# Optimization experiments

Measured on AMD Instinct MI355X. Metric: run time of the kernel, lower is better.

Reference implementation:

```python
import jax, jax.numpy as jnp
import numpy as np
import math

B, T_IN, T_COND, D, H, W = 2, 2048, 1024, 1024, 16, 512
HD = D // H
NEG = -1e9


def setup_inputs() -> dict:
    key = jax.random.key(0)
    ks = jax.random.split(key, 6)
    scale = 0.02
    x = jax.random.normal(ks[0], (B, T_IN, D), dtype=jnp.float32)
    condition = jax.random.normal(ks[1], (B, T_COND, D), dtype=jnp.float32)
    end_inds = jax.random.randint(ks[2], (B,), W, min(T_IN, T_COND), dtype=jnp.int32)
    in_proj_w = jax.random.normal(ks[3], (3 * D, D), dtype=jnp.float32) * scale
    in_proj_b = jnp.zeros((3 * D,), dtype=jnp.float32)
    out_w = jax.random.normal(ks[4], (D, D), dtype=jnp.float32) * scale
    out_b = jnp.zeros((D,), dtype=jnp.float32)
    return {"x": x, "condition": condition, "end_inds": end_inds,
            "in_proj_w": in_proj_w, "in_proj_b": in_proj_b,
            "out_w": out_w, "out_b": out_b}


def _window_mask(end_inds, t_in, t_cond):
    # allowed keys: index in [end - W, end) within each of the two segments
    e = end_inds[:, None].astype(jnp.int32)
    idx_in = jnp.arange(t_in, dtype=jnp.int32)[None, :]
    idx_c = jnp.arange(t_cond, dtype=jnp.int32)[None, :]
    m_in = (idx_in >= e - W) & (idx_in < e)
    m_c = (idx_c >= e - W) & (idx_c < e)
    return jnp.concatenate([m_in, m_c], axis=1)  # (B, S)


def reference(x, condition, end_inds, in_proj_w, in_proj_b, out_w, out_b):
    inp = jnp.concatenate([x, condition], axis=1)          # (B, S, D)
    S = inp.shape[1]
    qkv = inp @ in_proj_w.T + in_proj_b                     # (B, S, 3D)
    q, k, v = jnp.split(qkv, 3, axis=-1)
    # (B, H, S, HD)
    q = q.reshape(B, S, H, HD).transpose(0, 2, 1, 3)
    k = k.reshape(B, S, H, HD).transpose(0, 2, 1, 3)
    v = v.reshape(B, S, H, HD).transpose(0, 2, 1, 3)
    scores = jnp.einsum('bhqd,bhkd->bhqk', q, k) / math.sqrt(HD)
    mask = _window_mask(end_inds, x.shape[1], condition.shape[1])  # (B, S)
    scores = jnp.where(mask[:, None, None, :], scores, NEG)
    attn = jax.nn.softmax(scores, axis=-1)
    out = jnp.einsum('bhqk,bhkd->bhqd', attn, v)            # (B, H, S, HD)
    out = out.transpose(0, 2, 1, 3).reshape(B, S, D)
    return out @ out_w.T + out_b
```

## Files before the change

kernel.cpp:

```cpp
#include <hip/hip_runtime.h>
#include <stdint.h>

#define TIN   2048
#define TCOND 1024
#define SEQ   3072
#define NB    2
#define NH    16
#define DM    1024
#define HDIM  64
#define WIN   512
#define MROWS (NB*SEQ)
#define NQKV  (3*DM)

typedef float  floatx4 __attribute__((ext_vector_type(4)));
typedef short  bf16x8  __attribute__((ext_vector_type(8)));

__device__ __forceinline__ unsigned short f2bf(float f) {
    unsigned int u = __float_as_uint(f);
    u += 0x7fffu + ((u >> 16) & 1u);
    return (unsigned short)(u >> 16);
}

__device__ __forceinline__ unsigned int pack2bf(float a, float b) {
    return (unsigned int)f2bf(a) | ((unsigned int)f2bf(b) << 16);
}

__device__ __forceinline__ void gl2lds16(const void* g, void* l) {
    __builtin_amdgcn_global_load_lds(
        (const __attribute__((address_space(1))) unsigned int*)g,
        (__attribute__((address_space(3))) unsigned int*)l, 16, 0, 0);
}

__global__ __launch_bounds__(256) void pack_inp(const float* __restrict__ x,
                                                const float* __restrict__ cond,
                                                unsigned short* __restrict__ inp) {
    int v = blockIdx.x * 256 + threadIdx.x;
    int m  = v >> 8;
    int d4 = v & 255;
    int bb = (m >= SEQ) ? 1 : 0;
    int s  = m - bb * SEQ;
    const float* src = (s < TIN)
        ? x    + ((size_t)(bb * TIN   + s)        ) * DM + d4 * 4
        : cond + ((size_t)(bb * TCOND + (s - TIN))) * DM + d4 * 4;
    float4 f = *(const float4*)src;
    ushort4 u;
    u.x = f2bf(f.x); u.y = f2bf(f.y); u.z = f2bf(f.z); u.w = f2bf(f.w);
    *(ushort4*)(inp + (size_t)v * 4) = u;
}

__global__ __launch_bounds__(256) void cast_w(const float* __restrict__ w_in,
                                              const float* __restrict__ w_out,
                                              unsigned short* __restrict__ wi_bf,
                                              unsigned short* __restrict__ wo_bf) {
    int v = blockIdx.x * 256 + threadIdx.x;
    const float* src; unsigned short* dst; int idx;
    if (v < 786432) { src = w_in;  dst = wi_bf; idx = v; }
    else            { src = w_out; dst = wo_bf; idx = v - 786432; }
    float4 f = *(const float4*)(src + (size_t)idx * 4);
    ushort4 u;
    u.x = f2bf(f.x); u.y = f2bf(f.y); u.z = f2bf(f.z); u.w = f2bf(f.w);
    *(ushort4*)(dst + (size_t)idx * 4) = u;
}

template<int EPI>
__global__ __launch_bounds__(256) void gemm_bt(
        const unsigned short* __restrict__ A, const unsigned short* __restrict__ Bt,
        int M, int N, int K,
        const float* __restrict__ bias,
        unsigned short* __restrict__ q_ws, unsigned short* __restrict__ k_ws,
        unsigned short* __restrict__ vt_ws, float* __restrict__ outp) {
    __shared__ unsigned short smem[2 * 128 * 64];
    unsigned short* As = smem;
    unsigned short* Bs = smem + 128 * 64;
    const int tid  = threadIdx.x;
    const int wave = tid >> 6, lane = tid & 63;
    const int quad = lane >> 4, c16 = lane & 15;
    const int wr = wave >> 1, wc = wave & 1;
    const int m0 = blockIdx.y * 128, n0 = blockIdx.x * 128;

    floatx4 acc[4][4];
#pragma unroll
    for (int i = 0; i < 4; i++)
#pragma unroll
        for (int j = 0; j < 4; j++) acc[i][j] = (floatx4){0.f, 0.f, 0.f, 0.f};

    for (int k0 = 0; k0 < K; k0 += 64) {
        __syncthreads();
#pragma unroll
        for (int i = 0; i < 4; i++) {
            int flat = i * 256 + tid;
            int pr = flat >> 3, cp = flat & 7;
            gl2lds16(A + (size_t)(m0 + pr) * K + k0 + ((cp ^ (pr & 7)) << 3),
                     &As[(i * 256 + wave * 64) * 8]);
        }
#pragma unroll
        for (int i = 0; i < 4; i++) {
            int flat = i * 256 + tid;
            int pr = flat >> 3, cp = flat & 7;
            gl2lds16(Bt + (size_t)(n0 + pr) * K + k0 + ((cp ^ (pr & 7)) << 3),
                     &Bs[(i * 256 + wave * 64) * 8]);
        }
        __syncthreads();
#pragma unroll
        for (int kk = 0; kk < 2; kk++) {
            bf16x8 af[4], bfr[4];
#pragma unroll
            for (int t = 0; t < 4; t++) {
                int ra = wr * 64 + t * 16 + c16;
                int rb = wc * 64 + t * 16 + c16;
                af[t]  = *(const bf16x8*)&As[ra * 64 + (((kk * 4 + quad) ^ (ra & 7)) << 3)];
                bfr[t] = *(const bf16x8*)&Bs[rb * 64 + (((kk * 4 + quad) ^ (rb & 7)) << 3)];
            }
#pragma unroll
            for (int mt = 0; mt < 4; mt++)
#pragma unroll
                for (int nt = 0; nt < 4; nt++)
                    acc[mt][nt] = __builtin_amdgcn_mfma_f32_16x16x32_bf16(
                        af[mt], bfr[nt], acc[mt][nt], 0, 0, 0);
        }
    }

    if (EPI == 0) {
        const int which = n0 >> 10;
        const int h0 = (n0 >> 6) & 15;
        if (which == 2) {
#pragma unroll
            for (int mt = 0; mt < 4; mt++) {
                int m = m0 + wr * 64 + mt * 16 + quad * 4;
                int bb = (m >= SEQ) ? 1 : 0;
                int s = m - bb * SEQ;
#pragma unroll
                for (int nt = 0; nt < 4; nt++) {
                    int gn = n0 + wc * 64 + nt * 16 + c16;
                    float bi = bias[gn];
                    int h = (gn >> 6) & 15, hd = gn & 63;
                    uint2 w;
                    w.x = pack2bf(acc[mt][nt][0] + bi, acc[mt][nt][1] + bi);
                    w.y = pack2bf(acc[mt][nt][2] + bi, acc[mt][nt][3] + bi);
                    *(uint2*)&vt_ws[((size_t)(bb * NH + h) * HDIM + hd) * SEQ + s] = w;
                }
            }
        } else {
            unsigned short* dstb = (which == 0) ? q_ws : k_ws;
            const float qs = (which == 0) ? 0.125f : 1.0f;
#pragma unroll
            for (int mt = 0; mt < 4; mt++) {
                __syncthreads();
#pragma unroll
                for (int nt = 0; nt < 4; nt++) {
                    int col = wc * 64 + nt * 16 + c16;
                    float bi = bias[n0 + col];
#pragma unroll
                    for (int r = 0; r < 4; r++)
                        smem[(wr * 16 + quad * 4 + r) * 136 + col] =
                            f2bf((acc[mt][nt][r] + bi) * qs);
                }
                __syncthreads();
#pragma unroll
                for (int p = 0; p < 2; p++) {
                    int flat = p * 256 + tid;
                    int row = flat >> 4, seg = flat & 15;
                    bf16x8 v = *(const bf16x8*)&smem[row * 136 + seg * 8];
                    int m = m0 + (row >> 4) * 64 + mt * 16 + (row & 15);
                    int bb = (m >= SEQ) ? 1 : 0;
                    int s = m - bb * SEQ;
                    int h = h0 + (seg >> 3);
                    *(bf16x8*)&dstb[((size_t)(bb * NH + h) * SEQ + s) * HDIM + (seg & 7) * 8] = v;
                }
            }
        }
    } else {
        float* smf = (float*)smem;
#pragma unroll
        for (int mt = 0; mt < 4; mt++) {
            __syncthreads();
#pragma unroll
            for (int nt = 0; nt < 4; nt++) {
                int col = wc * 64 + nt * 16 + c16;
                float bi = bias[n0 + col];
#pragma unroll
                for (int r = 0; r < 4; r++)
                    smf[(wr * 16 + quad * 4 + r) * 132 + col] = acc[mt][nt][r] + bi;
            }
            __syncthreads();
#pragma unroll
            for (int p = 0; p < 4; p++) {
                int flat = p * 256 + tid;
                int row = flat >> 5, seg = flat & 31;
                float4 v = *(const float4*)&smf[row * 132 + seg * 4];
                int m = m0 + (row >> 4) * 64 + mt * 16 + (row & 15);
                *(float4*)&outp[(size_t)m * DM + n0 + seg * 4] = v;
            }
        }
    }
}

__global__ __launch_bounds__(256, 2) void attn_kernel(
        const unsigned short* __restrict__ Q, const unsigned short* __restrict__ K,
        const unsigned short* __restrict__ Vt, const int* __restrict__ end_inds,
        unsigned short* __restrict__ O) {
    __shared__ unsigned short smem[128 * 64 + 64 * 128];
    unsigned short* Ks = smem;
    unsigned short* Vs = smem + 128 * 64;

    const int tid  = threadIdx.x;
    const int wave = tid >> 6, lane = tid & 63;
    const int quad = lane >> 4, c16 = lane & 15;
    const int qt = blockIdx.x, h = blockIdx.y, b = blockIdx.z;
    const int bh = b * NH + h;
    const int e  = end_inds[b];
    const int qbase = qt * 192 + wave * 48;

    const unsigned short* Qp = Q + ((size_t)bh * SEQ + qbase) * HDIM;
    bf16x8 bq[3][2];
#pragma unroll
    for (int qi = 0; qi < 3; qi++)
#pragma unroll
        for (int kk = 0; kk < 2; kk++)
            bq[qi][kk] = *(const bf16x8*)&Qp[(qi * 16 + c16) * HDIM + kk * 32 + quad * 8];

    float l_run[3] = {0.f, 0.f, 0.f};
    floatx4 accO[3][4];
#pragma unroll
    for (int qi = 0; qi < 3; qi++)
#pragma unroll
        for (int t = 0; t < 4; t++) accO[qi][t] = (floatx4){0.f, 0.f, 0.f, 0.f};

    for (int ch = 0; ch < 8; ch++) {
        int s0 = (ch < 4) ? (e - WIN + ch * 128) : (TIN + e - WIN + (ch - 4) * 128);
        const unsigned short* Kc = K  + ((size_t)bh * SEQ + s0) * HDIM;
        const unsigned short* Vc = Vt + ((size_t)bh * HDIM) * SEQ + s0;
        __syncthreads();
#pragma unroll
        for (int i = 0; i < 4; i++) {
            int flat = i * 256 + tid;
            int pr = flat >> 3, cp = flat & 7;
            int m5 = pr & 31;
            int kl = (pr & ~31) + (((m5 & 15) >> 2) << 3) + (m5 & 3) + ((m5 >> 4) << 2);
            gl2lds16(Kc + kl * HDIM + ((cp ^ (pr & 7)) << 3), &Ks[(i * 256 + wave * 64) * 8]);
        }
#pragma unroll
        for (int i = 0; i < 4; i++) {
            int flat = i * 256 + tid;
            int row = flat >> 4, cp = flat & 15;
            gl2lds16(Vc + (size_t)row * SEQ + ((cp ^ (row & 15)) << 3),
                     &Vs[(i * 256 + wave * 64) * 8]);
        }
        __syncthreads();

#pragma unroll
        for (int u = 0; u < 4; u++) {
            unsigned int pb[3][4];
#pragma unroll
            for (int sub = 0; sub < 2; sub++) {
                int prow = u * 32 + sub * 16 + c16;
                int sw = c16 & 7;
                bf16x8 ka0 = *(const bf16x8*)&Ks[prow * 64 + (( quad      ^ sw) << 3)];
                bf16x8 ka1 = *(const bf16x8*)&Ks[prow * 64 + (((quad + 4) ^ sw) << 3)];
#pragma unroll
                for (int qi = 0; qi < 3; qi++) {
                    floatx4 z = (floatx4){0.f, 0.f, 0.f, 0.f};
                    z = __builtin_amdgcn_mfma_f32_16x16x32_bf16(ka0, bq[qi][0], z, 0, 0, 0);
                    z = __builtin_amdgcn_mfma_f32_16x16x32_bf16(ka1, bq[qi][1], z, 0, 0, 0);
                    float p0 = __expf(z[0]), p1 = __expf(z[1]);
                    float p2 = __expf(z[2]), p3 = __expf(z[3]);
                    l_run[qi] += (p0 + p1) + (p2 + p3);
                    pb[qi][sub * 2 + 0] = pack2bf(p0, p1);
                    pb[qi][sub * 2 + 1] = pack2bf(p2, p3);
                }
            }
#pragma unroll
            for (int t = 0; t < 4; t++) {
                bf16x8 va = *(const bf16x8*)&Vs[(t * 16 + c16) * 128 +
                                                (((u * 4 + quad) ^ c16) << 3)];
#pragma unroll
                for (int qi = 0; qi < 3; qi++)
                    accO[qi][t] = __builtin_amdgcn_mfma_f32_16x16x32_bf16(
                        va, *(const bf16x8*)&pb[qi][0], accO[qi][t], 0, 0, 0);
            }
        }
    }

    float inv[3];
#pragma unroll
    for (int qi = 0; qi < 3; qi++) {
        float l = l_run[qi];
        l += __shfl_xor(l, 16, 64);
        l += __shfl_xor(l, 32, 64);
        inv[qi] = 1.f / l;
    }

    __syncthreads();
    unsigned short* Os = smem + wave * (48 * 72);
#pragma unroll
    for (int qi = 0; qi < 3; qi++)
#pragma unroll
        for (int t = 0; t < 4; t++) {
            uint2 w;
            w.x = pack2bf(accO[qi][t][0] * inv[qi], accO[qi][t][1] * inv[qi]);
            w.y = pack2bf(accO[qi][t][2] * inv[qi], accO[qi][t][3] * inv[qi]);
            *(uint2*)&Os[(qi * 16 + c16) * 72 + t * 16 + quad * 4] = w;
        }
    __syncthreads();
#pragma unroll
    for (int pass = 0; pass < 6; pass++) {
        int rq = pass * 8 + (lane >> 3);
        int part = lane & 7;
        bf16x8 v = *(const bf16x8*)&Os[rq * 72 + part * 8];
        int s = qbase + rq;
        *(bf16x8*)&O[((size_t)b * SEQ + s) * DM + h * HDIM + part * 8] = v;
    }
}

extern "C" void kernel_launch(void* const* d_in, const int* in_sizes, int n_in,
                              void* d_out, int out_size, void* d_ws, size_t ws_size,
                              hipStream_t stream) {
    const float* x      = (const float*)d_in[0];
    const float* cond   = (const float*)d_in[1];
    const int*   e_inds = (const int*)d_in[2];
    const float* w_in   = (const float*)d_in[3];
    const float* b_in   = (const float*)d_in[4];
    const float* w_out  = (const float*)d_in[5];
    const float* b_out  = (const float*)d_in[6];
    float* out = (float*)d_out;

    char* ws = (char*)d_ws;
    unsigned short* inp_bf = (unsigned short*)(ws);
    unsigned short* wi_bf  = (unsigned short*)(ws + 12582912);
    unsigned short* wo_bf  = (unsigned short*)(ws + 18874368);
    unsigned short* q_ws   = (unsigned short*)(ws + 20971520);
    unsigned short* k_ws   = (unsigned short*)(ws + 33554432);
    unsigned short* vt_ws  = (unsigned short*)(ws + 46137344);
    unsigned short* o_bf   = inp_bf;

    pack_inp<<<6144, 256, 0, stream>>>(x, cond, inp_bf);
    cast_w<<<4096, 256, 0, stream>>>(w_in, w_out, wi_bf, wo_bf);
    gemm_bt<0><<<dim3(NQKV / 128, MROWS / 128), 256, 0, stream>>>(
        inp_bf, wi_bf, MROWS, NQKV, DM, b_in, q_ws, k_ws, vt_ws, nullptr);
    attn_kernel<<<dim3(SEQ / 192, NH, NB), 256, 0, stream>>>(
        q_ws, k_ws, vt_ws, e_inds, o_bf);
    gemm_bt<1><<<dim3(DM / 128, MROWS / 128), 256, 0, stream>>>(
        o_bf, wo_bf, MROWS, DM, DM, b_out, nullptr, nullptr, nullptr, out);
}
```

Before: 225.8 us.

## Double-buffer LDS tiles in GEMM and attention, merge cast kernels

The GEMM main loop becomes double-buffered with a K-tile of 32 instead of 64. The next tile's global-to-LDS loads are issued before computing on the current buffer, with one barrier per iteration and a new swizzle for the narrower rows. The attention kernel likewise double-buffers its K/V chunks, raising LDS use to 64KB per block, and precomputes load offsets outside the loop. The two fp32-to-bf16 cast kernels are merged into one launch. The aim is to hide global load latency behind MFMA work. The risks are that the compiler may insert conservative vmcnt waits that cancel the overlap, that the smaller GEMM K-tile doubles the number of barriers, and that the larger LDS footprint may limit occupancy.

```diff
diff --git a/kernel.cpp b/kernel.cpp
--- a/kernel.cpp
+++ b/kernel.cpp
@@ -31,35 +31,36 @@
         (__attribute__((address_space(3))) unsigned int*)l, 16, 0, 0);
 }
 
-__global__ __launch_bounds__(256) void pack_inp(const float* __restrict__ x,
-                                                const float* __restrict__ cond,
-                                                unsigned short* __restrict__ inp) {
-    int v = blockIdx.x * 256 + threadIdx.x;
-    int m  = v >> 8;
-    int d4 = v & 255;
-    int bb = (m >= SEQ) ? 1 : 0;
-    int s  = m - bb * SEQ;
-    const float* src = (s < TIN)
-        ? x    + ((size_t)(bb * TIN   + s)        ) * DM + d4 * 4
-        : cond + ((size_t)(bb * TCOND + (s - TIN))) * DM + d4 * 4;
-    float4 f = *(const float4*)src;
-    ushort4 u;
-    u.x = f2bf(f.x); u.y = f2bf(f.y); u.z = f2bf(f.z); u.w = f2bf(f.w);
-    *(ushort4*)(inp + (size_t)v * 4) = u;
-}
-
-__global__ __launch_bounds__(256) void cast_w(const float* __restrict__ w_in,
-                                              const float* __restrict__ w_out,
-                                              unsigned short* __restrict__ wi_bf,
-                                              unsigned short* __restrict__ wo_bf) {
-    int v = blockIdx.x * 256 + threadIdx.x;
-    const float* src; unsigned short* dst; int idx;
-    if (v < 786432) { src = w_in;  dst = wi_bf; idx = v; }
-    else            { src = w_out; dst = wo_bf; idx = v - 786432; }
-    float4 f = *(const float4*)(src + (size_t)idx * 4);
-    ushort4 u;
-    u.x = f2bf(f.x); u.y = f2bf(f.y); u.z = f2bf(f.z); u.w = f2bf(f.w);
-    *(ushort4*)(dst + (size_t)idx * 4) = u;
+__global__ __launch_bounds__(256) void prep(const float* __restrict__ x,
+                                            const float* __restrict__ cond,
+                                            const float* __restrict__ w_in,
+                                            const float* __restrict__ w_out,
+                                            unsigned short* __restrict__ inp,
+                                            unsigned short* __restrict__ wi_bf,
+                                            unsigned short* __restrict__ wo_bf) {
+    if (blockIdx.x < 6144) {
+        int v = blockIdx.x * 256 + threadIdx.x;
+        int m  = v >> 8;
+        int d4 = v & 255;
+        int bb = (m >= SEQ) ? 1 : 0;
+        int s  = m - bb * SEQ;
+        const float* src = (s < TIN)
+            ? x    + ((size_t)(bb * TIN   + s)        ) * DM + d4 * 4
+            : cond + ((size_t)(bb * TCOND + (s - TIN))) * DM + d4 * 4;
+        float4 f = *(const float4*)src;
+        ushort4 u;
+        u.x = f2bf(f.x); u.y = f2bf(f.y); u.z = f2bf(f.z); u.w = f2bf(f.w);
+        *(ushort4*)(inp + (size_t)v * 4) = u;
+    } else {
+        int v = (blockIdx.x - 6144) * 256 + threadIdx.x;
+        const float* src; unsigned short* dst; int idx;
+        if (v < 786432) { src = w_in;  dst = wi_bf; idx = v; }
+        else            { src = w_out; dst = wo_bf; idx = v - 786432; }
+        float4 f = *(const float4*)(src + (size_t)idx * 4);
+        ushort4 u;
+        u.x = f2bf(f.x); u.y = f2bf(f.y); u.z = f2bf(f.z); u.w = f2bf(f.w);
+        *(ushort4*)(dst + (size_t)idx * 4) = u;
+    }
 }
 
 template<int EPI>
@@ -69,55 +70,66 @@
         const float* __restrict__ bias,
         unsigned short* __restrict__ q_ws, unsigned short* __restrict__ k_ws,
         unsigned short* __restrict__ vt_ws, float* __restrict__ outp) {
-    __shared__ unsigned short smem[2 * 128 * 64];
-    unsigned short* As = smem;
-    unsigned short* Bs = smem + 128 * 64;
+    __shared__ unsigned short smem[2 * 8192];
     const int tid  = threadIdx.x;
     const int wave = tid >> 6, lane = tid & 63;
     const int quad = lane >> 4, c16 = lane & 15;
     const int wr = wave >> 1, wc = wave & 1;
     const int m0 = blockIdx.y * 128, n0 = blockIdx.x * 128;
 
+    const unsigned short* gA[2];
+    const unsigned short* gB[2];
+    int ldst[2];
+#pragma unroll
+    for (int i = 0; i < 2; i++) {
+        int flat = i * 256 + tid;
+        int pr = flat >> 2, cp = flat & 3;
+        int gc = cp ^ ((pr >> 1) & 3);
+        gA[i] = A  + (size_t)(m0 + pr) * K + (gc << 3);
+        gB[i] = Bt + (size_t)(n0 + pr) * K + (gc << 3);
+        ldst[i] = (i * 256 + wave * 64) * 8;
+    }
+
     floatx4 acc[4][4];
 #pragma unroll
     for (int i = 0; i < 4; i++)
 #pragma unroll
         for (int j = 0; j < 4; j++) acc[i][j] = (floatx4){0.f, 0.f, 0.f, 0.f};
 
-    for (int k0 = 0; k0 < K; k0 += 64) {
+    const int NIT = K >> 5;
+#pragma unroll
+    for (int i = 0; i < 2; i++) {
+        gl2lds16(gA[i], &smem[ldst[i]]);
+        gl2lds16(gB[i], &smem[4096 + ldst[i]]);
+    }
+
+    for (int it = 0; it < NIT; ++it) {
         __syncthreads();
-#pragma unroll
-        for (int i = 0; i < 4; i++) {
-            int flat = i * 256 + tid;
-            int pr = flat >> 3, cp = flat & 7;
-            gl2lds16(A + (size_t)(m0 + pr) * K + k0 + ((cp ^ (pr & 7)) << 3),
-                     &As[(i * 256 + wave * 64) * 8]);
-        }
-#pragma unroll
-        for (int i = 0; i < 4; i++) {
-            int flat = i * 256 + tid;
-            int pr = flat >> 3, cp = flat & 7;
-            gl2lds16(Bt + (size_t)(n0 + pr) * K + k0 + ((cp ^ (pr & 7)) << 3),
-                     &Bs[(i * 256 + wave * 64) * 8]);
-        }
-        __syncthreads();
-#pragma unroll
-        for (int kk = 0; kk < 2; kk++) {
-            bf16x8 af[4], bfr[4];
-#pragma unroll
-            for (int t = 0; t < 4; t++) {
-                int ra = wr * 64 + t * 16 + c16;
-                int rb = wc * 64 + t * 16 + c16;
-                af[t]  = *(const bf16x8*)&As[ra * 64 + (((kk * 4 + quad) ^ (ra & 7)) << 3)];
-                bfr[t] = *(const bf16x8*)&Bs[rb * 64 + (((kk * 4 + quad) ^ (rb & 7)) << 3)];
-            }
-#pragma unroll
-            for (int mt = 0; mt < 4; mt++)
-#pragma unroll
-                for (int nt = 0; nt < 4; nt++)
-                    acc[mt][nt] = __builtin_amdgcn_mfma_f32_16x16x32_bf16(
-                        af[mt], bfr[nt], acc[mt][nt], 0, 0, 0);
-        }
+        if (it + 1 < NIT) {
+            int buf = (it + 1) & 1;
+            int k0 = (it + 1) << 5;
+#pragma unroll
+            for (int i = 0; i < 2; i++) {
+                gl2lds16(gA[i] + k0, &smem[buf * 8192 + ldst[i]]);
+                gl2lds16(gB[i] + k0, &smem[buf * 8192 + 4096 + ldst[i]]);
+            }
+        }
+        const unsigned short* As = &smem[(it & 1) * 8192];
+        const unsigned short* Bs = As + 4096;
+        bf16x8 af[4], bfr[4];
+#pragma unroll
+        for (int t = 0; t < 4; t++) {
+            int ra = wr * 64 + t * 16 + c16;
+            int rb = wc * 64 + t * 16 + c16;
+            af[t]  = *(const bf16x8*)&As[ra * 32 + ((quad ^ ((ra >> 1) & 3)) << 3)];
+            bfr[t] = *(const bf16x8*)&Bs[rb * 32 + ((quad ^ ((rb >> 1) & 3)) << 3)];
+        }
+#pragma unroll
+        for (int mt = 0; mt < 4; mt++)
+#pragma unroll
+            for (int nt = 0; nt < 4; nt++)
+                acc[mt][nt] = __builtin_amdgcn_mfma_f32_16x16x32_bf16(
+                    af[mt], bfr[nt], acc[mt][nt], 0, 0, 0);
     }
 
     if (EPI == 0) {
@@ -199,9 +211,7 @@
         const unsigned short* __restrict__ Q, const unsigned short* __restrict__ K,
         const unsigned short* __restrict__ Vt, const int* __restrict__ end_inds,
         unsigned short* __restrict__ O) {
-    __shared__ unsigned short smem[128 * 64 + 64 * 128];
-    unsigned short* Ks = smem;
-    unsigned short* Vs = smem + 128 * 64;
+    __shared__ unsigned short smem[2 * 16384];
 
     const int tid  = threadIdx.x;
     const int wave = tid >> 6, lane = tid & 63;
@@ -226,27 +236,48 @@
 #pragma unroll
         for (int t = 0; t < 4; t++) accO[qi][t] = (floatx4){0.f, 0.f, 0.f, 0.f};
 
+    int k_pr[4], k_src[4], v_src[4], dst_off[4];
+#pragma unroll
+    for (int i = 0; i < 4; i++) {
+        int flat = i * 256 + tid;
+        int pr = flat >> 3, cp = flat & 7;
+        int m5 = pr & 31;
+        int kl = (pr & ~31) + (((m5 & 15) >> 2) << 3) + (m5 & 3) + ((m5 >> 4) << 2);
+        k_pr[i]  = pr;
+        k_src[i] = kl * HDIM + ((cp ^ (pr & 7)) << 3);
+        int vrow = flat >> 4, vcp = flat & 15;
+        v_src[i] = vrow * SEQ + ((vcp ^ (vrow & 15)) << 3);
+        dst_off[i] = (i * 256 + wave * 64) * 8;
+    }
+
+    const unsigned short* Kbase = K  + (size_t)bh * SEQ * HDIM;
+    const unsigned short* Vbase = Vt + (size_t)bh * HDIM * SEQ;
+
+    {
+        int s0 = e - WIN;
+#pragma unroll
+        for (int i = 0; i < 4; i++) {
+            gl2lds16(Kbase + (size_t)s0 * HDIM + k_src[i], &smem[dst_off[i]]);
+            gl2lds16(Vbase + s0 + v_src[i], &smem[8192 + dst_off[i]]);
+        }
+    }
+
     for (int ch = 0; ch < 8; ch++) {
-        int s0 = (ch < 4) ? (e - WIN + ch * 128) : (TIN + e - WIN + (ch - 4) * 128);
-        const unsigned short* Kc = K  + ((size_t)bh * SEQ + s0) * HDIM;
-        const unsigned short* Vc = Vt + ((size_t)bh * HDIM) * SEQ + s0;
         __syncthreads();
-#pragma unroll
-        for (int i = 0; i < 4; i++) {
-            int flat = i * 256 + tid;
-            int pr = flat >> 3, cp = flat & 7;
-            int m5 = pr & 31;
-            int kl = (pr & ~31) + (((m5 & 15) >> 2) << 3) + (m5 & 3) + ((m5 >> 4) << 2);
-            gl2lds16(Kc + kl * HDIM + ((cp ^ (pr & 7)) << 3), &Ks[(i * 256 + wave * 64) * 8]);
-        }
-#pragma unroll
-        for (int i = 0; i < 4; i++) {
-            int flat = i * 256 + tid;
-            int row = flat >> 4, cp = flat & 15;
-            gl2lds16(Vc + (size_t)row * SEQ + ((cp ^ (row & 15)) << 3),
-                     &Vs[(i * 256 + wave * 64) * 8]);
-        }
-        __syncthreads();
+        if (ch + 1 < 8) {
+            int buf = (ch + 1) & 1;
+            int cn = ch + 1;
+            int s0 = (cn < 4) ? (e - WIN + cn * 128) : (TIN + e - WIN + (cn - 4) * 128);
+#pragma unroll
+            for (int i = 0; i < 4; i++) {
+                gl2lds16(Kbase + (size_t)s0 * HDIM + k_src[i],
+                         &smem[buf * 16384 + dst_off[i]]);
+                gl2lds16(Vbase + s0 + v_src[i],
+                         &smem[buf * 16384 + 8192 + dst_off[i]]);
+            }
+        }
+        const unsigned short* Ks = &smem[(ch & 1) * 16384];
+        const unsigned short* Vs = Ks + 8192;
 
 #pragma unroll
         for (int u = 0; u < 4; u++) {
@@ -333,8 +364,7 @@
     unsigned short* vt_ws  = (unsigned short*)(ws + 46137344);
     unsigned short* o_bf   = inp_bf;
 
-    pack_inp<<<6144, 256, 0, stream>>>(x, cond, inp_bf);
-    cast_w<<<4096, 256, 0, stream>>>(w_in, w_out, wi_bf, wo_bf);
+    prep<<<10240, 256, 0, stream>>>(x, cond, w_in, w_out, inp_bf, wi_bf, wo_bf);
     gemm_bt<0><<<dim3(NQKV / 128, MROWS / 128), 256, 0, stream>>>(
         inp_bf, wi_bf, MROWS, NQKV, DM, b_in, q_ws, k_ws, vt_ws, nullptr);
     attn_kernel<<<dim3(SEQ / 192, NH, NB), 256, 0, stream>>>(
```

New measurement: 221.9 us. About the same (-1.7%).
